# Optimization experiments

Hardware: AMD Instinct MI355X
Metric: run time of the kernel (lower is better)

Reference implementation:

```python
import jax, jax.numpy as jnp
import numpy as np

B, A, C, M = 8, 98304, 80, 32
ALPHA, GAMMA = 0.25, 2.0


def setup_inputs() -> dict:
    key = jax.random.key(0)
    k1, k2, k3, k4, k5, k6, k7, k8 = jax.random.split(key, 8)
    classifications = jax.random.uniform(k1, (B, A, C), dtype=jnp.float32)
    regressions = jax.random.normal(k2, (B, A, 4), dtype=jnp.float32)
    # valid anchor boxes inside a 640px image
    ax = jax.random.uniform(k3, (A,)) * 512.0
    ay = jax.random.uniform(k4, (A,)) * 512.0
    aw = jax.random.uniform(k5, (A, 2)) * 120.0 + 8.0
    anchors = jnp.stack([ax, ay, ax + aw[:, 0], ay + aw[:, 1]], axis=-1)[None].astype(jnp.float32)
    # valid GT boxes with class labels in [0, C) (no -1 padding: all annotations valid)
    gx = jax.random.uniform(k6, (B, M, 2)) * 480.0
    gw = jax.random.uniform(k7, (B, M, 2)) * 150.0 + 10.0
    gcls = jax.random.randint(k8, (B, M), 0, C).astype(jnp.float32)
    annotations = jnp.concatenate([gx, gx + gw, gcls[..., None]], axis=-1).astype(jnp.float32)
    return {
        "classifications": classifications,
        "regressions": regressions,
        "anchors": anchors,
        "annotations": annotations,
        "negative_iou_thr": 0.4,
        "positive_iou_thr": 0.5,
    }


def calc_iou(a, b):
    # a: [A,4] anchors, b: [M,4] gt boxes -> [A,M]
    area = (b[:, 2] - b[:, 0]) * (b[:, 3] - b[:, 1])
    iw = jnp.clip(jnp.minimum(a[:, 2:3], b[:, 2]) - jnp.maximum(a[:, 0:1], b[:, 0]), 0.0)
    ih = jnp.clip(jnp.minimum(a[:, 3:4], b[:, 3]) - jnp.maximum(a[:, 1:2], b[:, 1]), 0.0)
    inter = iw * ih
    ua = jnp.clip(((a[:, 2] - a[:, 0]) * (a[:, 3] - a[:, 1]))[:, None] + area - inter, 1e-8)
    return inter / ua


def focal_loss(classifications, regressions, anchors, annotations, negative_iou_thr, positive_iou_thr):
    anchor = anchors[0]  # [A,4]
    aw = anchor[:, 2] - anchor[:, 0]
    ah = anchor[:, 3] - anchor[:, 1]
    acx = anchor[:, 0] + 0.5 * aw
    acy = anchor[:, 1] + 0.5 * ah

    def per_image(classification, regression, annot):
        p = jnp.clip(classification, 1e-4, 1.0 - 1e-4)
        valid = annot[:, 4] != -1.0  # [M] (all valid in test data)
        iou = jnp.where(valid[None, :], calc_iou(anchor, annot[:, :4]), -1.0)  # [A,M]
        iou_max = jnp.max(iou, axis=1)
        iou_arg = jnp.argmax(iou, axis=1)
        assigned = annot[iou_arg]  # [A,5]

        pos = iou_max >= positive_iou_thr  # [A]
        num_pos = jnp.sum(pos.astype(jnp.float32))
        onehot = jax.nn.one_hot(assigned[:, 4].astype(jnp.int32), C, dtype=jnp.float32)
        # targets: 1 for assigned class on positives, 0 elsewhere on pos/neg anchors, -1 ignored
        targets = jnp.where(pos[:, None], onehot,
                            jnp.where((iou_max < negative_iou_thr)[:, None], 0.0, -1.0))

        is_one = targets == 1.0
        alpha_factor = jnp.where(is_one, ALPHA, 1.0 - ALPHA)
        focal_w = alpha_factor * jnp.where(is_one, 1.0 - p, p) ** GAMMA
        bce = -(targets * jnp.log(p) + (1.0 - targets) * jnp.log(1.0 - p))
        cls_loss = jnp.where(targets != -1.0, focal_w * bce, 0.0)
        cls_loss = jnp.sum(cls_loss) / jnp.clip(num_pos, 1.0)

        gw = jnp.clip(assigned[:, 2] - assigned[:, 0], None, None)
        gh = assigned[:, 3] - assigned[:, 1]
        gcx = assigned[:, 0] + 0.5 * gw
        gcy = assigned[:, 1] + 0.5 * gh
        gw = jnp.clip(gw, 1.0)
        gh = jnp.clip(gh, 1.0)
        t = jnp.stack([(gcx - acx) / aw, (gcy - acy) / ah,
                       jnp.log(gw / aw), jnp.log(gh / ah)], axis=1)
        t = t / jnp.array([0.1, 0.1, 0.2, 0.2], dtype=jnp.float32)
        diff = jnp.abs(t - regression)
        sl1 = jnp.where(diff <= 1.0 / 9.0, 0.5 * 9.0 * diff * diff, diff - 0.5 / 9.0)
        reg_loss = jnp.sum(jnp.where(pos[:, None], sl1, 0.0)) / jnp.clip(num_pos * 4.0, 1.0)
        return cls_loss, reg_loss

    cls_l, reg_l = jax.vmap(per_image)(classifications, regressions, annotations)
    return jnp.mean(cls_l).reshape(1), jnp.mean(reg_l).reshape(1)


def reference(classifications, regressions, anchors, annotations, negative_iou_thr, positive_iou_thr):
    return focal_loss(classifications, regressions, anchors, annotations,
                      negative_iou_thr, positive_iou_thr)
```

## Files before the change

kernel.cpp:

```cpp
#include <hip/hip_runtime.h>

#define B_ 8
#define A_ 98304
#define C_ 80
#define M_ 32
#define BLK 256

__device__ __forceinline__ float focal_term(float praw, bool is_one) {
    float p = fminf(fmaxf(praw, 1e-4f), 1.0f - 1e-4f);
    float q = is_one ? p : (1.0f - p);
    float a = is_one ? 0.25f : 0.75f;
    float om = 1.0f - q;
    return a * om * om * (-__logf(q));
}

__device__ __forceinline__ float smooth_l1(float t, float r) {
    float d = fabsf(t - r);
    return (d <= (1.0f / 9.0f)) ? (0.5f * 9.0f * d * d) : (d - 0.5f / 9.0f);
}

__global__ __launch_bounds__(BLK) void focal_main(
    const float* __restrict__ cls,
    const float* __restrict__ regr,
    const float* __restrict__ anchors,
    const float* __restrict__ ann,
    const float* __restrict__ neg_thr_p,
    const float* __restrict__ pos_thr_p,
    float* __restrict__ acc)
{
    __shared__ float s_ann[M_ * 5];
    __shared__ int   s_state[BLK];
    __shared__ float s_red[(BLK / 64) * 3];

    const int tid = threadIdx.x;
    const int blocksPerImg = A_ / BLK;
    const int b  = blockIdx.x / blocksPerImg;
    const int a0 = (blockIdx.x % blocksPerImg) * BLK;

    if (tid < M_ * 5) s_ann[tid] = ann[b * M_ * 5 + tid];
    __syncthreads();

    const float neg_thr = neg_thr_p[0];
    const float pos_thr = pos_thr_p[0];

    const int a = a0 + tid;
    const float4 an = reinterpret_cast<const float4*>(anchors)[a];
    const float aw = an.z - an.x;
    const float ah = an.w - an.y;
    const float areaA = aw * ah;

    float iou_max = -1e30f;
    int   arg = 0;
#pragma unroll
    for (int m = 0; m < M_; ++m) {
        const float bx0 = s_ann[m * 5 + 0];
        const float by0 = s_ann[m * 5 + 1];
        const float bx1 = s_ann[m * 5 + 2];
        const float by1 = s_ann[m * 5 + 3];
        const float areaB = (bx1 - bx0) * (by1 - by0);
        const float iw = fmaxf(fminf(an.z, bx1) - fmaxf(an.x, bx0), 0.0f);
        const float ih = fmaxf(fminf(an.w, by1) - fmaxf(an.y, by0), 0.0f);
        const float inter = iw * ih;
        const float ua = fmaxf(areaA + areaB - inter, 1e-8f);
        float iou = inter / ua;
        if (s_ann[m * 5 + 4] == -1.0f) iou = -1.0f;
        if (iou > iou_max) { iou_max = iou; arg = m; }
    }

    const bool pos = (iou_max >= pos_thr);
    const bool neg = (iou_max <  neg_thr);

    float reg_partial = 0.0f;
    float pos_count   = 0.0f;
    int   state       = -1;
    if (pos) {
        const float gx0 = s_ann[arg * 5 + 0];
        const float gy0 = s_ann[arg * 5 + 1];
        const float gx1 = s_ann[arg * 5 + 2];
        const float gy1 = s_ann[arg * 5 + 3];
        state = (int)s_ann[arg * 5 + 4];
        pos_count = 1.0f;

        float gw = gx1 - gx0;
        float gh = gy1 - gy0;
        const float gcx = gx0 + 0.5f * gw;
        const float gcy = gy0 + 0.5f * gh;
        gw = fmaxf(gw, 1.0f);
        gh = fmaxf(gh, 1.0f);
        const float acx = an.x + 0.5f * aw;
        const float acy = an.y + 0.5f * ah;

        const float t0 = ((gcx - acx) / aw) / 0.1f;
        const float t1 = ((gcy - acy) / ah) / 0.1f;
        const float t2 = logf(gw / aw) / 0.2f;
        const float t3 = logf(gh / ah) / 0.2f;

        const float4 r = reinterpret_cast<const float4*>(regr)[(size_t)b * A_ + a];
        reg_partial = smooth_l1(t0, r.x) + smooth_l1(t1, r.y) +
                      smooth_l1(t2, r.z) + smooth_l1(t3, r.w);
    } else if (neg) {
        state = -2;
    }
    s_state[tid] = state;
    __syncthreads();

    const float4* cls4 = reinterpret_cast<const float4*>(
        cls + ((size_t)b * A_ + a0) * C_);
    float cls_partial = 0.0f;
#pragma unroll 4
    for (int it = 0; it < (BLK * C_ / 4) / BLK; ++it) {
        const int vid  = it * BLK + tid;
        const float4 v = cls4[vid];
        const int eidx = vid * 4;
        const int al   = eidx / C_;
        const int c0   = eidx - al * C_;
        const int st   = s_state[al];
        if (st != -1) {
            cls_partial += focal_term(v.x, st == c0);
            cls_partial += focal_term(v.y, st == c0 + 1);
            cls_partial += focal_term(v.z, st == c0 + 2);
            cls_partial += focal_term(v.w, st == c0 + 3);
        }
    }

#pragma unroll
    for (int off = 32; off > 0; off >>= 1) {
        cls_partial += __shfl_down(cls_partial, off);
        reg_partial += __shfl_down(reg_partial, off);
        pos_count   += __shfl_down(pos_count,   off);
    }
    const int wave = tid >> 6;
    if ((tid & 63) == 0) {
        s_red[wave * 3 + 0] = cls_partial;
        s_red[wave * 3 + 1] = reg_partial;
        s_red[wave * 3 + 2] = pos_count;
    }
    __syncthreads();
    if (tid == 0) {
        float c = 0.0f, r = 0.0f, n = 0.0f;
#pragma unroll
        for (int w = 0; w < BLK / 64; ++w) {
            c += s_red[w * 3 + 0];
            r += s_red[w * 3 + 1];
            n += s_red[w * 3 + 2];
        }
        atomicAdd(&acc[b * 3 + 0], c);
        atomicAdd(&acc[b * 3 + 1], r);
        atomicAdd(&acc[b * 3 + 2], n);
    }
}

__global__ void focal_finalize(const float* __restrict__ acc, float* __restrict__ out) {
    const int t = threadIdx.x;
    float cls_l = 0.0f, reg_l = 0.0f;
    if (t < B_) {
        const float np = acc[t * 3 + 2];
        cls_l = acc[t * 3 + 0] / fmaxf(np, 1.0f);
        reg_l = acc[t * 3 + 1] / fmaxf(np * 4.0f, 1.0f);
    }
#pragma unroll
    for (int off = 32; off > 0; off >>= 1) {
        cls_l += __shfl_down(cls_l, off);
        reg_l += __shfl_down(reg_l, off);
    }
    if (t == 0) {
        out[0] = cls_l / (float)B_;
        out[1] = reg_l / (float)B_;
    }
}

extern "C" void kernel_launch(void* const* d_in, const int* in_sizes, int n_in,
                              void* d_out, int out_size, void* d_ws, size_t ws_size,
                              hipStream_t stream) {
    const float* cls     = (const float*)d_in[0];
    const float* regr    = (const float*)d_in[1];
    const float* anchors = (const float*)d_in[2];
    const float* ann     = (const float*)d_in[3];
    const float* negt    = (const float*)d_in[4];
    const float* post    = (const float*)d_in[5];
    float* acc = (float*)d_ws;

    hipMemsetAsync(acc, 0, B_ * 3 * sizeof(float), stream);
    focal_main<<<B_ * (A_ / BLK), BLK, 0, stream>>>(cls, regr, anchors, ann,
                                                    negt, post, acc);
    focal_finalize<<<1, 64, 0, stream>>>(acc, (float*)d_out);
}
```

Before: 131.3 us.

## Compute focal loss densely as negative term with per-anchor positive correction

The classification loop now applies the negative focal term uniformly to every class element, scaled by a per-anchor weight held in shared memory. Each positive anchor adds a correction for its single target class, computed separately by one gather load. This removes the per-element class comparisons and selects from the hot loop. IoU argmax is done by cross-multiplication instead of division, annotations are stored as SoA with precomputed areas, and log2 with a folded constant replaces ln; threshold comparisons by cross-multiplication may round slightly differently at the boundaries.

```diff
diff --git a/kernel.cpp b/kernel.cpp
--- a/kernel.cpp
+++ b/kernel.cpp
@@ -6,12 +6,11 @@
 #define M_ 32
 #define BLK 256
 
-__device__ __forceinline__ float focal_term(float praw, bool is_one) {
-    float p = fminf(fmaxf(praw, 1e-4f), 1.0f - 1e-4f);
-    float q = is_one ? p : (1.0f - p);
-    float a = is_one ? 0.25f : 0.75f;
-    float om = 1.0f - q;
-    return a * om * om * (-__logf(q));
+#define NEGC (-0.75f * 0.69314718055994531f)
+
+__device__ __forceinline__ float neg_u(float praw) {
+    const float p = fminf(fmaxf(praw, 1e-4f), 1.0f - 1e-4f);
+    return p * p * __log2f(1.0f - p);
 }
 
 __device__ __forceinline__ float smooth_l1(float t, float r) {
@@ -28,8 +27,8 @@
     const float* __restrict__ pos_thr_p,
     float* __restrict__ acc)
 {
-    __shared__ float s_ann[M_ * 5];
-    __shared__ int   s_state[BLK];
+    __shared__ float s_x0[M_], s_y0[M_], s_x1[M_], s_y1[M_], s_ab[M_], s_cls[M_];
+    __shared__ float s_w[BLK];
     __shared__ float s_red[(BLK / 64) * 3];
 
     const int tid = threadIdx.x;
@@ -37,7 +36,13 @@
     const int b  = blockIdx.x / blocksPerImg;
     const int a0 = (blockIdx.x % blocksPerImg) * BLK;
 
-    if (tid < M_ * 5) s_ann[tid] = ann[b * M_ * 5 + tid];
+    if (tid < M_) {
+        const float* am = ann + ((size_t)b * M_ + tid) * 5;
+        const float x0 = am[0], y0 = am[1], x1 = am[2], y1 = am[3], cl = am[4];
+        s_x0[tid] = x0; s_y0[tid] = y0; s_x1[tid] = x1; s_y1[tid] = y1;
+        s_ab[tid] = (x1 - x0) * (y1 - y0);
+        s_cls[tid] = cl;
+    }
     __syncthreads();
 
     const float neg_thr = neg_thr_p[0];
@@ -49,37 +54,30 @@
     const float ah = an.w - an.y;
     const float areaA = aw * ah;
 
-    float iou_max = -1e30f;
+    float ib = -1.0f, ub = 1.0f;
     int   arg = 0;
 #pragma unroll
     for (int m = 0; m < M_; ++m) {
-        const float bx0 = s_ann[m * 5 + 0];
-        const float by0 = s_ann[m * 5 + 1];
-        const float bx1 = s_ann[m * 5 + 2];
-        const float by1 = s_ann[m * 5 + 3];
-        const float areaB = (bx1 - bx0) * (by1 - by0);
-        const float iw = fmaxf(fminf(an.z, bx1) - fmaxf(an.x, bx0), 0.0f);
-        const float ih = fmaxf(fminf(an.w, by1) - fmaxf(an.y, by0), 0.0f);
-        const float inter = iw * ih;
-        const float ua = fmaxf(areaA + areaB - inter, 1e-8f);
-        float iou = inter / ua;
-        if (s_ann[m * 5 + 4] == -1.0f) iou = -1.0f;
-        if (iou > iou_max) { iou_max = iou; arg = m; }
+        const float iw = fmaxf(fminf(an.z, s_x1[m]) - fmaxf(an.x, s_x0[m]), 0.0f);
+        const float ih = fmaxf(fminf(an.w, s_y1[m]) - fmaxf(an.y, s_y0[m]), 0.0f);
+        float inter = iw * ih;
+        const float ua = fmaxf(areaA + s_ab[m] - inter, 1e-8f);
+        if (s_cls[m] == -1.0f) inter = -1.0f;
+        if (inter * ub > ib * ua) { ib = inter; ub = ua; arg = m; }
     }
-
-    const bool pos = (iou_max >= pos_thr);
-    const bool neg = (iou_max <  neg_thr);
+    const bool pos = (ib >= pos_thr * ub);
+    const bool neg = (ib <  neg_thr * ub);
 
     float reg_partial = 0.0f;
     float pos_count   = 0.0f;
-    int   state       = -1;
+    float cls_corr    = 0.0f;
+    float cw = (pos || neg) ? NEGC : 0.0f;
+
     if (pos) {
-        const float gx0 = s_ann[arg * 5 + 0];
-        const float gy0 = s_ann[arg * 5 + 1];
-        const float gx1 = s_ann[arg * 5 + 2];
-        const float gy1 = s_ann[arg * 5 + 3];
-        state = (int)s_ann[arg * 5 + 4];
         pos_count = 1.0f;
+        const float gx0 = s_x0[arg], gy0 = s_y0[arg];
+        const float gx1 = s_x1[arg], gy1 = s_y1[arg];
+        const int   kcls = (int)s_cls[arg];
 
         float gw = gx1 - gx0;
         float gh = gy1 - gy0;
@@ -89,38 +87,35 @@
         gh = fmaxf(gh, 1.0f);
         const float acx = an.x + 0.5f * aw;
         const float acy = an.y + 0.5f * ah;
-
-        const float t0 = ((gcx - acx) / aw) / 0.1f;
-        const float t1 = ((gcy - acy) / ah) / 0.1f;
-        const float t2 = logf(gw / aw) / 0.2f;
-        const float t3 = logf(gh / ah) / 0.2f;
-
+        const float t0 = ((gcx - acx) / aw) * 10.0f;
+        const float t1 = ((gcy - acy) / ah) * 10.0f;
+        const float t2 = logf(gw / aw) * 5.0f;
+        const float t3 = logf(gh / ah) * 5.0f;
         const float4 r = reinterpret_cast<const float4*>(regr)[(size_t)b * A_ + a];
         reg_partial = smooth_l1(t0, r.x) + smooth_l1(t1, r.y) +
                       smooth_l1(t2, r.z) + smooth_l1(t3, r.w);
-    } else if (neg) {
-        state = -2;
+
+        const float praw = cls[((size_t)b * A_ + a) * C_ + kcls];
+        const float p  = fminf(fmaxf(praw, 1e-4f), 1.0f - 1e-4f);
+        const float om = 1.0f - p;
+        const float negv = neg_u(praw) * NEGC;
+        const float posv = 0.25f * om * om * (-__logf(p));
+        cls_corr = posv - negv;
     }
-    s_state[tid] = state;
+    s_w[tid] = cw;
     __syncthreads();
 
     const float4* cls4 = reinterpret_cast<const float4*>(
         cls + ((size_t)b * A_ + a0) * C_);
-    float cls_partial = 0.0f;
-#pragma unroll 4
+    float cls_partial = cls_corr;
+#pragma unroll 5
     for (int it = 0; it < (BLK * C_ / 4) / BLK; ++it) {
-        const int vid  = it * BLK + tid;
+        const int vid = it * BLK + tid;
         const float4 v = cls4[vid];
-        const int eidx = vid * 4;
-        const int al   = eidx / C_;
-        const int c0   = eidx - al * C_;
-        const int st   = s_state[al];
-        if (st != -1) {
-            cls_partial += focal_term(v.x, st == c0);
-            cls_partial += focal_term(v.y, st == c0 + 1);
-            cls_partial += focal_term(v.z, st == c0 + 2);
-            cls_partial += focal_term(v.w, st == c0 + 3);
-        }
+        const int al = vid / 20;
+        const float cw2 = s_w[al];
+        const float u = (neg_u(v.x) + neg_u(v.y)) + (neg_u(v.z) + neg_u(v.w));
+        cls_partial = fmaf(u, cw2, cls_partial);
     }
 
 #pragma unroll
```

Measured after the change: 117.5 us. 10.5% less time.
